# Kernel tuning notes

Measured on AMD Instinct MI355X. Metric: run time of the kernel, lower is better.

Reference implementation:

```python
import jax, jax.numpy as jnp
import numpy as np

B, S, N_STATE, N_HEAD = 8, 4096, 1024, 16
H_DIM = N_STATE // N_HEAD           # 64
NUM_ROT = H_DIM // 2                # 32
BASE = 10000.0


def setup_inputs() -> dict:
    key = jax.random.key(0)
    k0, k1, k2 = jax.random.split(key, 3)
    x = jax.random.normal(k0, (B, S, N_STATE), dtype=jnp.float32)
    thetas = 0.1 * jax.random.normal(k1, (NUM_ROT,), dtype=jnp.float32)
    rotation_pairs = jax.random.uniform(k2, (NUM_ROT, 2), dtype=jnp.float32) * H_DIM
    theta_scale = jnp.ones((1,), dtype=jnp.float32)
    # orthogonal init, mirroring reset_parameters()
    q, _ = np.linalg.qr(np.random.RandomState(0).randn(H_DIM, H_DIM))
    rotation_matrix = jnp.asarray(q, dtype=jnp.float32)
    inv_freq = 1.0 / (BASE ** (jnp.arange(0, H_DIM, 2, dtype=jnp.float32) / H_DIM))
    return {"x": x, "thetas": thetas, "rotation_pairs": rotation_pairs,
            "theta_scale": theta_scale, "rotation_matrix": rotation_matrix,
            "inv_freq": inv_freq}


def reference(x, thetas, rotation_pairs, theta_scale, rotation_matrix, inv_freq):
    b, s, n_state = x.shape
    h_dim = rotation_matrix.shape[0]
    n_head = n_state // h_dim

    # rotation_pairs[k].long() in torch -> truncation toward zero (values >= 0)
    idx = rotation_pairs.astype(jnp.int32)

    # Compose all Givens rotations into one h_dim x h_dim matrix (tiny),
    # instead of num_rotations full matmuls against x.
    # math.cos/math.sin in the torch code detach theta -> stop_gradient.
    thetas_scaled = jax.lax.stop_gradient(thetas * theta_scale[0])

    def step(R, inputs):
        i, j, theta = inputs
        c, sn = jnp.cos(theta), jnp.sin(theta)
        G = jnp.eye(h_dim, dtype=x.dtype)
        # same assignment order as torch (handles i == j overwrite identically)
        G = G.at[i, i].set(c).at[i, j].set(-sn).at[j, i].set(sn).at[j, j].set(c)
        return R @ G, None

    R, _ = jax.lax.scan(step, jnp.eye(h_dim, dtype=x.dtype),
                        (idx[:, 0], idx[:, 1], thetas_scaled))
    M = R @ rotation_matrix                       # [h_dim, h_dim]

    xh = x.reshape(b, s, n_head, h_dim)
    xr = jnp.einsum('bshd,de->bshe', xh, M)       # learned rotation

    pos = jnp.arange(s, dtype=x.dtype)            # [s]
    sinusoid = pos[:, None] * inv_freq[None, :]   # [s, h_dim//2]
    sin = jnp.sin(sinusoid)[None, :, None, :]
    cos = jnp.cos(sinusoid)[None, :, None, :]

    x1, x2 = xr[..., 0::2], xr[..., 1::2]
    out = jnp.concatenate([x1 * cos - x2 * sin, x1 * sin + x2 * cos], axis=-1)
    return out.reshape(b, s, n_state)
```

## Files before the change

kernel.cpp:

```cpp
#include <hip/hip_runtime.h>

#define S_      4096
#define NROT    32
#define NCHUNK  32768
#define NBLK    2048
#define WPB     4
#define NWAVE   (NBLK * WPB)
#define NITER   (NCHUNK / NWAVE)
#define MST     68

typedef __bf16 bf16x4 __attribute__((ext_vector_type(4)));
typedef __bf16 bf16x8 __attribute__((ext_vector_type(8)));
typedef float  f32x4  __attribute__((ext_vector_type(4)));
typedef unsigned short ushort_t;

__device__ __forceinline__ int swzb(int a) { return a ^ (((a >> 7) & 7) << 4); }

union Scratch {
    float    M[64][MST];
    ushort_t frag[4096];
    float    chunk[WPB][512];
};

__global__ __launch_bounds__(256) void rope_fused_kernel(
    const float* __restrict__ x,
    const float* __restrict__ thetas,
    const float* __restrict__ rot_pairs,
    const float* __restrict__ theta_scale,
    const float* __restrict__ rot_matrix,
    const float* __restrict__ inv_freq,
    float* __restrict__ out)
{
    __shared__ __align__(16) Scratch sc;
    __shared__ float trig[NROT][2];
    __shared__ int   ipair[NROT][2];

    const int t    = threadIdx.x;
    const int lane = t & 63;
    const int w    = t >> 6;
    const int l15  = lane & 15;
    const int lhi  = lane >> 4;
    const int u    = l15 >> 1;
    const bool even = (lane & 1) == 0;

    const int c0 = blockIdx.x * WPB + w;

    f32x4 q[4];
    {
        const float* xa = x + (size_t)c0 * 1024 + lane * 4;
        #pragma unroll
        for (int k = 0; k < 4; ++k)
            q[k] = *reinterpret_cast<const f32x4*>(xa + k * 256);
    }

    {
        const int row = t >> 2, c4 = (t & 3) * 16;
        const float* src = rot_matrix + row * 64 + c4;
        #pragma unroll
        for (int j = 0; j < 4; ++j)
            *reinterpret_cast<f32x4*>(&sc.M[row][c4 + 4 * j]) =
                *reinterpret_cast<const f32x4*>(src + 4 * j);
    }
    if (t < NROT) {
        const float th = thetas[t] * theta_scale[0];
        trig[t][0]  = cosf(th);
        trig[t][1]  = sinf(th);
        ipair[t][0] = (int)rot_pairs[2 * t];
        ipair[t][1] = (int)rot_pairs[2 * t + 1];
    }
    __syncthreads();

    if (t < 64) {
        #pragma unroll
        for (int k = NROT - 1; k >= 0; --k) {
            const int   i = ipair[k][0];
            const int   j = ipair[k][1];
            const float c = trig[k][0];
            const float s = trig[k][1];
            const float mi = sc.M[i][t];
            const float mj = sc.M[j][t];
            if (i == j) {
                sc.M[i][t] = c * mi;
            } else {
                sc.M[i][t] = fmaf(c, mi, -s * mj);
                sc.M[j][t] = fmaf(s, mi,  c * mj);
            }
        }
    }
    __syncthreads();

    float vals[16];
    #pragma unroll
    for (int m = 0; m < 16; ++m) {
        const int F  = t * 16 + m;
        const int f  = F >> 9;
        const int ln = (F >> 3) & 63;
        const int i  = F & 7;
        const int kt = f >> 2, nt = f & 3;
        const int d  = kt * 32 + 8 * (ln >> 4) + i;
        const int n  = ln & 15;
        const int e  = 8 * (n >> 1) + 2 * nt + (n & 1);
        vals[m] = sc.M[d][e];
    }
    __syncthreads();

    {
        uint32_t dw[8];
        #pragma unroll
        for (int m = 0; m < 8; ++m) {
            union { __bf16 h; ushort_t s; } lo, hi;
            lo.h = (__bf16)vals[2 * m];
            hi.h = (__bf16)vals[2 * m + 1];
            dw[m] = (uint32_t)lo.s | ((uint32_t)hi.s << 16);
        }
        uint32_t* dst = reinterpret_cast<uint32_t*>(sc.frag + t * 16);
        *reinterpret_cast<uint4*>(dst)     = make_uint4(dw[0], dw[1], dw[2], dw[3]);
        *reinterpret_cast<uint4*>(dst + 4) = make_uint4(dw[4], dw[5], dw[6], dw[7]);
    }
    __syncthreads();

    bf16x8 bf[2][4];
    #pragma unroll
    for (int kt = 0; kt < 2; ++kt)
        #pragma unroll
        for (int nt = 0; nt < 4; ++nt)
            bf[kt][nt] = *reinterpret_cast<const bf16x8*>(
                sc.frag + ((kt * 4 + nt) * 512 + lane * 8));
    __syncthreads();

    const f32x4 invf = *reinterpret_cast<const f32x4*>(inv_freq + 4 * u);
    const float INV2PI = 0.15915494309189535f;
    char* wbuf = reinterpret_cast<char*>(sc.chunk[w]);

    int wr_off[4];
    #pragma unroll
    for (int k = 0; k < 4; ++k)
        wr_off[k] = swzb((k * 4 + lhi) * 128 + l15 * 8);
    const int rd0 = swzb(l15 * 128 + lhi * 16);
    const int rd1 = swzb(l15 * 128 + lhi * 16 + 64);

    int c = c0;
    #pragma unroll 1
    for (int it = 0; it < NITER; ++it) {
        #pragma unroll
        for (int k = 0; k < 4; ++k) {
            bf16x4 h;
            #pragma unroll
            for (int i = 0; i < 4; ++i) h[i] = (__bf16)q[k][i];
            *reinterpret_cast<bf16x4*>(wbuf + wr_off[k]) = h;
        }

        if (it + 1 < NITER) {
            const float* xn = x + (size_t)(c + NWAVE) * 1024 + lane * 4;
            #pragma unroll
            for (int k = 0; k < 4; ++k)
                q[k] = *reinterpret_cast<const f32x4*>(xn + k * 256);
        }

        const bf16x8 a0 = *reinterpret_cast<const bf16x8*>(wbuf + rd0);
        const bf16x8 a1 = *reinterpret_cast<const bf16x8*>(wbuf + rd1);

        f32x4 acc[4];
        #pragma unroll
        for (int nt = 0; nt < 4; ++nt) {
            acc[nt] = (f32x4){0.f, 0.f, 0.f, 0.f};
            acc[nt] = __builtin_amdgcn_mfma_f32_16x16x32_bf16(a0, bf[0][nt], acc[nt], 0, 0, 0);
            acc[nt] = __builtin_amdgcn_mfma_f32_16x16x32_bf16(a1, bf[1][nt], acc[nt], 0, 0, 0);
        }

        const int s = c & (S_ - 1);
        float cs[4], sn2[4];
        #pragma unroll
        for (int nt = 0; nt < 4; ++nt) {
            float rev = (float)s * invf[nt] * INV2PI;
            rev -= floorf(rev);
            const float sv = __builtin_amdgcn_sinf(rev);
            cs[nt]  = __builtin_amdgcn_cosf(rev);
            sn2[nt] = even ? -sv : sv;
        }

        float* outc = out + (size_t)c * 1024;
        #pragma unroll
        for (int j = 0; j < 4; ++j) {
            f32x4 res;
            #pragma unroll
            for (int nt = 0; nt < 4; ++nt) {
                const float own = acc[nt][j];
                const float oth = __shfl_xor(own, 1, 64);
                res[nt] = fmaf(oth, sn2[nt], own * cs[nt]);
            }
            const int row  = lhi * 4 + j;
            const int col0 = (even ? 0 : 32) + 4 * u;
            __builtin_nontemporal_store(
                res, reinterpret_cast<f32x4*>(outc + row * 64 + col0));
        }

        c += NWAVE;
    }
}

extern "C" void kernel_launch(void* const* d_in, const int* in_sizes, int n_in,
                              void* d_out, int out_size, void* d_ws, size_t ws_size,
                              hipStream_t stream)
{
    const float* x           = (const float*)d_in[0];
    const float* thetas      = (const float*)d_in[1];
    const float* rot_pairs   = (const float*)d_in[2];
    const float* theta_scale = (const float*)d_in[3];
    const float* rot_matrix  = (const float*)d_in[4];
    const float* inv_freq    = (const float*)d_in[5];
    float*       outp        = (float*)d_out;

    rope_fused_kernel<<<NBLK, 256, 0, stream>>>(
        x, thetas, rot_pairs, theta_scale, rot_matrix, inv_freq, outp);
}
```

Baseline: 49.27 us.

## Load A fragments directly from global, keep B in LDS, shrink grid

Each lane now loads its MFMA A-operand elements straight from global memory in fragment order and converts them to bf16 in registers, which removes the per-iteration LDS write/read staging of the x chunk. The B fragments are re-read from LDS every iteration instead of being held in 32 VGPRs, which frees registers. An opaque zero offset stops the compiler from hoisting those loads, and sched barriers pin the MFMA order. The grid shrinks to 1280 blocks with a grid-stride loop. The cost is that the software prefetch of the next chunk is dropped, and global loads become 32-byte strided pieces per lane rather than fully contiguous 1 KB rows.

New measurement: 50.03 us. No clear change (+1.5%).

```diff
diff --git a/kernel.cpp b/kernel.cpp
--- a/kernel.cpp
+++ b/kernel.cpp
@@ -3,23 +3,18 @@
 #define S_      4096
 #define NROT    32
 #define NCHUNK  32768
-#define NBLK    2048
+#define NBLK    1280
 #define WPB     4
 #define NWAVE   (NBLK * WPB)
-#define NITER   (NCHUNK / NWAVE)
 #define MST     68
 
-typedef __bf16 bf16x4 __attribute__((ext_vector_type(4)));
 typedef __bf16 bf16x8 __attribute__((ext_vector_type(8)));
 typedef float  f32x4  __attribute__((ext_vector_type(4)));
 typedef unsigned short ushort_t;
 
-__device__ __forceinline__ int swzb(int a) { return a ^ (((a >> 7) & 7) << 4); }
-
 union Scratch {
     float    M[64][MST];
     ushort_t frag[4096];
-    float    chunk[WPB][512];
 };
 
 __global__ __launch_bounds__(256) void rope_fused_kernel(
@@ -42,16 +37,6 @@
     const int lhi  = lane >> 4;
     const int u    = l15 >> 1;
     const bool even = (lane & 1) == 0;
-
-    const int c0 = blockIdx.x * WPB + w;
-
-    f32x4 q[4];
-    {
-        const float* xa = x + (size_t)c0 * 1024 + lane * 4;
-        #pragma unroll
-        for (int k = 0; k < 4; ++k)
-            q[k] = *reinterpret_cast<const f32x4*>(xa + k * 256);
-    }
 
     {
         const int row = t >> 2, c4 = (t & 3) * 16;
@@ -119,53 +104,41 @@
     }
     __syncthreads();
 
-    bf16x8 bf[2][4];
-    #pragma unroll
-    for (int kt = 0; kt < 2; ++kt)
-        #pragma unroll
-        for (int nt = 0; nt < 4; ++nt)
-            bf[kt][nt] = *reinterpret_cast<const bf16x8*>(
-                sc.frag + ((kt * 4 + nt) * 512 + lane * 8));
-    __syncthreads();
-
     const f32x4 invf = *reinterpret_cast<const f32x4*>(inv_freq + 4 * u);
     const float INV2PI = 0.15915494309189535f;
-    char* wbuf = reinterpret_cast<char*>(sc.chunk[w]);
+    const int   aoff   = l15 * 64 + lhi * 8;
+    const int   c0     = blockIdx.x * WPB + w;
 
-    int wr_off[4];
-    #pragma unroll
-    for (int k = 0; k < 4; ++k)
-        wr_off[k] = swzb((k * 4 + lhi) * 128 + l15 * 8);
-    const int rd0 = swzb(l15 * 128 + lhi * 16);
-    const int rd1 = swzb(l15 * 128 + lhi * 16 + 64);
+    #pragma unroll 1
+    for (int c = c0; c < NCHUNK; c += NWAVE) {
+        const float* xp = x + (size_t)c * 1024 + aoff;
+        const f32x4 q0 = *reinterpret_cast<const f32x4*>(xp);
+        const f32x4 q1 = *reinterpret_cast<const f32x4*>(xp + 4);
+        const f32x4 q2 = *reinterpret_cast<const f32x4*>(xp + 32);
+        const f32x4 q3 = *reinterpret_cast<const f32x4*>(xp + 36);
 
-    int c = c0;
-    #pragma unroll 1
-    for (int it = 0; it < NITER; ++it) {
+        bf16x8 a0, a1;
         #pragma unroll
-        for (int k = 0; k < 4; ++k) {
-            bf16x4 h;
-            #pragma unroll
-            for (int i = 0; i < 4; ++i) h[i] = (__bf16)q[k][i];
-            *reinterpret_cast<bf16x4*>(wbuf + wr_off[k]) = h;
+        for (int i = 0; i < 4; ++i) {
+            a0[i]     = (__bf16)q0[i];
+            a0[4 + i] = (__bf16)q1[i];
+            a1[i]     = (__bf16)q2[i];
+            a1[4 + i] = (__bf16)q3[i];
         }
 
-        if (it + 1 < NITER) {
-            const float* xn = x + (size_t)(c + NWAVE) * 1024 + lane * 4;
-            #pragma unroll
-            for (int k = 0; k < 4; ++k)
-                q[k] = *reinterpret_cast<const f32x4*>(xn + k * 256);
-        }
-
-        const bf16x8 a0 = *reinterpret_cast<const bf16x8*>(wbuf + rd0);
-        const bf16x8 a1 = *reinterpret_cast<const bf16x8*>(wbuf + rd1);
+        int opq;
+        asm volatile("v_mov_b32 %0, 0" : "=v"(opq));
+        const ushort_t* fr = sc.frag + opq + lane * 8;
 
         f32x4 acc[4];
         #pragma unroll
         for (int nt = 0; nt < 4; ++nt) {
+            const bf16x8 b0 = *reinterpret_cast<const bf16x8*>(fr + nt * 512);
+            const bf16x8 b1 = *reinterpret_cast<const bf16x8*>(fr + (4 + nt) * 512);
             acc[nt] = (f32x4){0.f, 0.f, 0.f, 0.f};
-            acc[nt] = __builtin_amdgcn_mfma_f32_16x16x32_bf16(a0, bf[0][nt], acc[nt], 0, 0, 0);
-            acc[nt] = __builtin_amdgcn_mfma_f32_16x16x32_bf16(a1, bf[1][nt], acc[nt], 0, 0, 0);
+            acc[nt] = __builtin_amdgcn_mfma_f32_16x16x32_bf16(a0, b0, acc[nt], 0, 0, 0);
+            acc[nt] = __builtin_amdgcn_mfma_f32_16x16x32_bf16(a1, b1, acc[nt], 0, 0, 0);
+            __builtin_amdgcn_sched_barrier(0);
         }
 
         const int s = c & (S_ - 1);
@@ -194,8 +167,6 @@
             __builtin_nontemporal_store(
                 res, reinterpret_cast<f32x4*>(outc + row * 64 + col0));
         }
-
-        c += NWAVE;
     }
 }
 
```
